# Kernel tuning notes

Measured on AMD Instinct MI355X. Metric: run time of the kernel, lower is better.

## Reference

```python
import jax, jax.numpy as jnp
import numpy as np

M = 150        # AR2 tail-fit window
LAM = 1e-3     # ridge regularizer in the 2x2 solve
CLIP_K = 4.0   # soft clip multiplier
H = 96         # forecast horizon (base_model.H)


def setup_inputs() -> dict:
    key = jax.random.key(0)
    k1, k2 = jax.random.split(key)
    x = jax.random.normal(k1, (32, 512, 2048), dtype=jnp.float32)
    W = jax.random.normal(k2, (2048, 96), dtype=jnp.float32) * 0.02
    return {"x": x, "W": W}


def _ar2_forecast(x):
    # x: (B, C, L); closed-form AR2 fit on last M samples, vectorized over (B, C)
    y = x[..., -M:]                     # (B, C, M)
    Y = y[..., 2:]                      # targets
    p1 = y[..., 1:-1]
    p2 = y[..., :-2]
    s = lambda a, b: jnp.sum(a * b, axis=-1)
    A11 = s(p1, p1) + LAM
    A22 = s(p2, p2) + LAM
    A12 = s(p1, p2)
    b1 = s(p1, Y)
    b2 = s(p2, Y)
    det = A11 * A22 - A12 * A12
    a1 = (b1 * A22 - b2 * A12) / det    # (B, C)
    a2 = (A11 * b2 - A12 * b1) / det

    def step(carry, _):
        y1, y2 = carry
        yn = a1 * y1 + a2 * y2
        return (yn, y1), yn

    _, out = jax.lax.scan(step, (x[..., -1], x[..., -2]), None, length=H)
    return jnp.moveaxis(out, 0, -1)     # (B, C, H)


def reference(x, W):
    # AR2 part is computed on detached history in the original (numpy round-trip)
    Yb = jax.lax.stop_gradient(_ar2_forecast(x))
    d_hat = jnp.einsum('bcl,lh->bch', x, W)          # base model: per-channel linear head
    y_hat = Yb + d_hat
    last = x[..., -1:]                               # (B, C, 1), broadcasts over H
    hstd = jnp.maximum(jnp.std(x, axis=-1, ddof=1, keepdims=True), 1e-6)  # torch unbiased std
    return jnp.clip(y_hat, last - CLIP_K * hstd, last + CLIP_K * hstd)
```

## Files before the change

kernel.cpp:

```cpp
#include <hip/hip_runtime.h>
#include <math.h>

constexpr int L     = 2048;
constexpr int NH    = 96;
constexpr int MLEN  = 150;
constexpr int NAR   = 148;
constexpr float LAM    = 0.001f;
constexpr float CLIP_K = 4.0f;

constexpr int TM     = 16;
constexpr int KM     = 64;
constexpr int MSTEPS = L / KM;
constexpr int NBUF   = 4;

typedef __attribute__((ext_vector_type(8))) short short8;
typedef __attribute__((ext_vector_type(4))) float floatx4;

__device__ inline short f2bf(float f) {
    union { float f; unsigned u; } v; v.f = f;
    unsigned r = v.u + 0x7FFFu + ((v.u >> 16) & 1u);
    return (short)(r >> 16);
}

__global__ __launch_bounds__(256) void wt_kernel(
    const float* __restrict__ W, short* __restrict__ Wt)
{
    int idx = blockIdx.x * 256 + threadIdx.x;
    int n = idx >> 11;
    int k = idx & 2047;
    Wt[idx] = f2bf(W[k * NH + n]);
}

__global__ __launch_bounds__(256, 4) void gemm_ar2_kernel(
    const float* __restrict__ x, const short* __restrict__ Wt,
    float* __restrict__ out)
{
    __shared__ float As[NBUF][TM * KM];
    __shared__ float arbuf[2][64][12];
    __shared__ float Ys[TM][NH + 1];
    __shared__ float los[TM], his[TM];
    __shared__ float s2[TM], q2[TM];

    const int t    = threadIdx.x;
    const int lane = t & 63;
    const int wv   = t >> 6;
    const int g    = wv & 1;
    const int e    = wv >> 1;
    const int m    = lane & 15;
    const int quad = lane >> 4;
    const int row0 = blockIdx.x * TM;

    const int rA = t >> 4, chA = t & 15;
    const float* pa = x + (size_t)(row0 + rA) * L
                        + ((chA >> 3) * 32 + ((chA & 7) ^ (rA & 7)) * 4);

    const short* pb0 = Wt + (size_t)(g * 48 + m) * L + e * 32 + quad * 8;
    const short* pb1 = pb0 + 16 * (size_t)L;
    const short* pb2 = pb0 + 32 * (size_t)L;

    floatx4 acc[3];
    #pragma unroll
    for (int jj = 0; jj < 3; ++jj) acc[jj] = floatx4{0.f, 0.f, 0.f, 0.f};
    float sum = 0.f, sumsq = 0.f;

    const int pA0  = (2 * quad)     ^ (m & 7);
    const int pA1  = (2 * quad + 1) ^ (m & 7);
    const int aoff = m * KM + e * 32;

    auto stageA = [&](int buf, int k0) {
        __builtin_amdgcn_global_load_lds(
            (const __attribute__((address_space(1))) unsigned int*)(pa + k0),
            (__attribute__((address_space(3))) unsigned int*)&As[buf][wv * 256], 16, 0, 0);
    };

    stageA(0, 0);
    asm volatile("" ::: "memory");
    short8 cb0 = *(const short8*)(pb0);
    short8 cb1 = *(const short8*)(pb1);
    short8 cb2 = *(const short8*)(pb2);
    asm volatile("" ::: "memory");
    stageA(1, KM);
    stageA(2, 2 * KM);

    #pragma unroll
    for (int s = 0; s < MSTEPS; ++s) {
        const int cur = s & 3;

        asm volatile("s_waitcnt vmcnt(5)" ::: "memory");
        __builtin_amdgcn_s_barrier();
        __builtin_amdgcn_sched_barrier(0);

        const int off = (s + 1 < MSTEPS ? s + 1 : s) * KM;
        short8 nb0 = *(const short8*)(pb0 + off);
        short8 nb1 = *(const short8*)(pb1 + off);
        short8 nb2 = *(const short8*)(pb2 + off);
        asm volatile("" ::: "memory");
        if (s + 3 < MSTEPS) stageA((s + 3) & 3, (s + 3) * KM);

        float4 f0 = *(const float4*)&As[cur][aoff + pA0 * 4];
        float4 f1 = *(const float4*)&As[cur][aoff + pA1 * 4];

        if (g == 0) {
            sum  += ((f0.x + f0.y) + (f0.z + f0.w))
                  + ((f1.x + f1.y) + (f1.z + f1.w));
            sumsq = fmaf(f0.x, f0.x, sumsq); sumsq = fmaf(f0.y, f0.y, sumsq);
            sumsq = fmaf(f0.z, f0.z, sumsq); sumsq = fmaf(f0.w, f0.w, sumsq);
            sumsq = fmaf(f1.x, f1.x, sumsq); sumsq = fmaf(f1.y, f1.y, sumsq);
            sumsq = fmaf(f1.z, f1.z, sumsq); sumsq = fmaf(f1.w, f1.w, sumsq);
        }

        short8 af;
        af[0] = f2bf(f0.x); af[1] = f2bf(f0.y); af[2] = f2bf(f0.z); af[3] = f2bf(f0.w);
        af[4] = f2bf(f1.x); af[5] = f2bf(f1.y); af[6] = f2bf(f1.z); af[7] = f2bf(f1.w);

        acc[0] = __builtin_amdgcn_mfma_f32_16x16x32_bf16(af, cb0, acc[0], 0, 0, 0);
        acc[1] = __builtin_amdgcn_mfma_f32_16x16x32_bf16(af, cb1, acc[1], 0, 0, 0);
        acc[2] = __builtin_amdgcn_mfma_f32_16x16x32_bf16(af, cb2, acc[2], 0, 0, 0);

        cb0 = nb0; cb1 = nb1; cb2 = nb2;
    }

    float* ar = &arbuf[0][0][0];
    if (e == 1) {
        #pragma unroll
        for (int jj = 0; jj < 3; ++jj)
            #pragma unroll
            for (int reg = 0; reg < 4; ++reg)
                ar[(g * 64 + lane) * 12 + jj * 4 + reg] = acc[jj][reg];
        if (g == 0) {
            float su = sum, sq = sumsq;
            su += __shfl_xor(su, 16); su += __shfl_xor(su, 32);
            sq += __shfl_xor(sq, 16); sq += __shfl_xor(sq, 32);
            if (quad == 0) { s2[m] = su; q2[m] = sq; }
        }
    }
    __syncthreads();

    if (e == 0) {
        #pragma unroll
        for (int jj = 0; jj < 3; ++jj)
            #pragma unroll
            for (int reg = 0; reg < 4; ++reg)
                acc[jj][reg] += ar[(g * 64 + lane) * 12 + jj * 4 + reg];

        if (g == 0) {
            sum   += __shfl_xor(sum,   16); sum   += __shfl_xor(sum,   32);
            sumsq += __shfl_xor(sumsq, 16); sumsq += __shfl_xor(sumsq, 32);

            const float* ytail = x + (size_t)(row0 + m) * L + (L - MLEN);
            float A11 = 0.f, A22 = 0.f, A12 = 0.f, b1 = 0.f, b2 = 0.f;
            for (int i = quad; i < NAR; i += 4) {
                float p2v = ytail[i];
                float p1v = ytail[i + 1];
                float Yv  = ytail[i + 2];
                A11 = fmaf(p1v, p1v, A11);
                A22 = fmaf(p2v, p2v, A22);
                A12 = fmaf(p1v, p2v, A12);
                b1  = fmaf(p1v, Yv,  b1);
                b2  = fmaf(p2v, Yv,  b2);
            }
            A11 += __shfl_xor(A11, 16); A11 += __shfl_xor(A11, 32);
            A22 += __shfl_xor(A22, 16); A22 += __shfl_xor(A22, 32);
            A12 += __shfl_xor(A12, 16); A12 += __shfl_xor(A12, 32);
            b1  += __shfl_xor(b1,  16); b1  += __shfl_xor(b1,  32);
            b2  += __shfl_xor(b2,  16); b2  += __shfl_xor(b2,  32);

            if (quad == 0) {
                sum   += s2[m];
                sumsq += q2[m];
                A11 += LAM; A22 += LAM;
                float det = A11 * A22 - A12 * A12;
                float a1c = (b1 * A22 - b2 * A12) / det;
                float a2c = (A11 * b2 - A12 * b1) / det;

                float last = ytail[MLEN - 1];
                float y1 = last;
                float y2 = ytail[MLEN - 2];
                for (int n = 0; n < NH; ++n) {
                    float yn = a1c * y1 + a2c * y2;
                    Ys[m][n] = yn;
                    y2 = y1; y1 = yn;
                }
                float var  = (sumsq - sum * sum * (1.0f / L)) * (1.0f / (L - 1));
                float hstd = fmaxf(sqrtf(fmaxf(var, 0.f)), 1e-6f);
                los[m] = last - CLIP_K * hstd;
                his[m] = last + CLIP_K * hstd;
            }
        }
    }
    __syncthreads();

    if (e == 0) {
        #pragma unroll
        for (int reg = 0; reg < 4; ++reg) {
            int rl = quad * 4 + reg;
            float lo = los[rl], hi = his[rl];
            #pragma unroll
            for (int jj = 0; jj < 3; ++jj) {
                int c = (3 * g + jj) * 16 + m;
                float v = acc[jj][reg] + Ys[rl][c];
                v = fminf(fmaxf(v, lo), hi);
                out[(size_t)(row0 + rl) * NH + c] = v;
            }
        }
    }
}

extern "C" void kernel_launch(void* const* d_in, const int* in_sizes, int n_in,
                              void* d_out, int out_size, void* d_ws, size_t ws_size,
                              hipStream_t stream) {
    const float* x = (const float*)d_in[0];
    const float* W = (const float*)d_in[1];
    float* out = (float*)d_out;
    short* Wt  = (short*)d_ws;

    wt_kernel<<<dim3((NH * L) / 256), dim3(256), 0, stream>>>(W, Wt);

    const int rows = 32 * 512;
    gemm_ar2_kernel<<<dim3(rows / TM), dim3(256), 0, stream>>>(x, Wt, out);
}
```

Baseline: 220.2 us.

## Replace LDS-staged A pipeline with direct global loads and K-halved wave split

```diff
diff --git a/kernel.cpp b/kernel.cpp
--- a/kernel.cpp
+++ b/kernel.cpp
@@ -9,9 +9,9 @@
 constexpr float CLIP_K = 4.0f;
 
 constexpr int TM     = 16;
-constexpr int KM     = 64;
-constexpr int MSTEPS = L / KM;
-constexpr int NBUF   = 4;
+constexpr int KH     = 1024;
+constexpr int KSTEP  = 32;
+constexpr int NSTEPS = KH / KSTEP;
 
 typedef __attribute__((ext_vector_type(8))) short short8;
 typedef __attribute__((ext_vector_type(4))) float floatx4;
@@ -31,11 +31,10 @@
     Wt[idx] = f2bf(W[k * NH + n]);
 }
 
-__global__ __launch_bounds__(256, 4) void gemm_ar2_kernel(
+__global__ void gemm_ar2_kernel(
     const float* __restrict__ x, const short* __restrict__ Wt,
     float* __restrict__ out)
 {
-    __shared__ float As[NBUF][TM * KM];
     __shared__ float arbuf[2][64][12];
     __shared__ float Ys[TM][NH + 1];
     __shared__ float los[TM], his[TM];
@@ -50,11 +49,8 @@
     const int quad = lane >> 4;
     const int row0 = blockIdx.x * TM;
 
-    const int rA = t >> 4, chA = t & 15;
-    const float* pa = x + (size_t)(row0 + rA) * L
-                        + ((chA >> 3) * 32 + ((chA & 7) ^ (rA & 7)) * 4);
-
-    const short* pb0 = Wt + (size_t)(g * 48 + m) * L + e * 32 + quad * 8;
+    const float* pa = x + (size_t)(row0 + m) * L + e * KH + quad * 8;
+    const short* pb0 = Wt + (size_t)(g * 48 + m) * L + e * KH + quad * 8;
     const short* pb1 = pb0 + 16 * (size_t)L;
     const short* pb2 = pb0 + 32 * (size_t)L;
 
@@ -63,42 +59,14 @@
     for (int jj = 0; jj < 3; ++jj) acc[jj] = floatx4{0.f, 0.f, 0.f, 0.f};
     float sum = 0.f, sumsq = 0.f;
 
-    const int pA0  = (2 * quad)     ^ (m & 7);
-    const int pA1  = (2 * quad + 1) ^ (m & 7);
-    const int aoff = m * KM + e * 32;
-
-    auto stageA = [&](int buf, int k0) {
-        __builtin_amdgcn_global_load_lds(
-            (const __attribute__((address_space(1))) unsigned int*)(pa + k0),
-            (__attribute__((address_space(3))) unsigned int*)&As[buf][wv * 256], 16, 0, 0);
-    };
-
-    stageA(0, 0);
-    asm volatile("" ::: "memory");
-    short8 cb0 = *(const short8*)(pb0);
-    short8 cb1 = *(const short8*)(pb1);
-    short8 cb2 = *(const short8*)(pb2);
-    asm volatile("" ::: "memory");
-    stageA(1, KM);
-    stageA(2, 2 * KM);
-
     #pragma unroll
-    for (int s = 0; s < MSTEPS; ++s) {
-        const int cur = s & 3;
-
-        asm volatile("s_waitcnt vmcnt(5)" ::: "memory");
-        __builtin_amdgcn_s_barrier();
-        __builtin_amdgcn_sched_barrier(0);
-
-        const int off = (s + 1 < MSTEPS ? s + 1 : s) * KM;
-        short8 nb0 = *(const short8*)(pb0 + off);
-        short8 nb1 = *(const short8*)(pb1 + off);
-        short8 nb2 = *(const short8*)(pb2 + off);
-        asm volatile("" ::: "memory");
-        if (s + 3 < MSTEPS) stageA((s + 3) & 3, (s + 3) * KM);
-
-        float4 f0 = *(const float4*)&As[cur][aoff + pA0 * 4];
-        float4 f1 = *(const float4*)&As[cur][aoff + pA1 * 4];
+    for (int s = 0; s < NSTEPS; ++s) {
+        const int off = s * KSTEP;
+        float4 f0 = *(const float4*)(pa + off);
+        float4 f1 = *(const float4*)(pa + off + 4);
+        short8 b0 = *(const short8*)(pb0 + off);
+        short8 b1 = *(const short8*)(pb1 + off);
+        short8 b2 = *(const short8*)(pb2 + off);
 
         if (g == 0) {
             sum  += ((f0.x + f0.y) + (f0.z + f0.w))
@@ -113,11 +81,9 @@
         af[0] = f2bf(f0.x); af[1] = f2bf(f0.y); af[2] = f2bf(f0.z); af[3] = f2bf(f0.w);
         af[4] = f2bf(f1.x); af[5] = f2bf(f1.y); af[6] = f2bf(f1.z); af[7] = f2bf(f1.w);
 
-        acc[0] = __builtin_amdgcn_mfma_f32_16x16x32_bf16(af, cb0, acc[0], 0, 0, 0);
-        acc[1] = __builtin_amdgcn_mfma_f32_16x16x32_bf16(af, cb1, acc[1], 0, 0, 0);
-        acc[2] = __builtin_amdgcn_mfma_f32_16x16x32_bf16(af, cb2, acc[2], 0, 0, 0);
-
-        cb0 = nb0; cb1 = nb1; cb2 = nb2;
+        acc[0] = __builtin_amdgcn_mfma_f32_16x16x32_bf16(af, b0, acc[0], 0, 0, 0);
+        acc[1] = __builtin_amdgcn_mfma_f32_16x16x32_bf16(af, b1, acc[1], 0, 0, 0);
+        acc[2] = __builtin_amdgcn_mfma_f32_16x16x32_bf16(af, b2, acc[2], 0, 0, 0);
     }
 
     float* ar = &arbuf[0][0][0];
```

Result: slower. 247.8 us (+12.5%).
